# Optimization experiments

Hardware: AMD Instinct MI355X
Metric: run time of the kernel (lower is better)

Reference implementation:

```python
import jax, jax.numpy as jnp
import numpy as np
from jax import lax

TAU = 1.0
HIDDEN = 512
OUT = 12
BATCH = 8192
STEPS = 256


def setup_inputs() -> dict:
    key = jax.random.key(0)
    k = jax.random.split(key, 6)
    scale = 1.0 / np.sqrt(HIDDEN)
    return {
        "x": jax.random.normal(k[0], (BATCH, 1), dtype=jnp.float32),
        "T": STEPS,
        "I_w": jax.random.normal(k[1], (HIDDEN, 1), dtype=jnp.float32) * scale,
        "H_w": jax.random.normal(k[2], (HIDDEN, HIDDEN), dtype=jnp.float32) * scale,
        "O_w": jax.random.normal(k[3], (OUT, HIDDEN), dtype=jnp.float32) * scale,
        "v": jax.random.normal(k[4], (HIDDEN,), dtype=jnp.float32) * 0.05,
        "m": jax.random.normal(k[5], (OUT,), dtype=jnp.float32) * 0.05,
    }


def reference(x, T, I_w, H_w, O_w, v, m):
    # x: [B, 1]; I_w: [H, 1]; H_w: [H, H]; O_w: [O, H]
    B = x.shape[0]
    H = H_w.shape[0]
    alpha = 1.0 / TAU
    # x is constant across timesteps, so precompute the input drive once.
    drive = x @ I_w.T + v  # [B, H]

    def step(carry, _):
        u, z = carry
        u = (1.0 - alpha) * u + alpha * (drive + z @ H_w.T)
        z = jnp.tanh(u)
        y = jax.nn.sigmoid(z @ O_w.T + m)  # [B, O]
        return (u, z), y

    u0 = jnp.zeros((B, H), dtype=x.dtype)
    z0 = jnp.zeros((B, H), dtype=x.dtype)
    _, Y = lax.scan(step, (u0, z0), None, length=T)  # Y: [T, B, O]
    return jnp.transpose(Y, (1, 0, 2))  # [B, T, O]
```

## Files before the change

### kernel.cpp

```cpp
#include <hip/hip_runtime.h>

typedef __attribute__((ext_vector_type(4)))  int   int32x4;
typedef __attribute__((ext_vector_type(16))) int   int32x16;
typedef __attribute__((ext_vector_type(16))) float f32x16;
typedef unsigned char uchar;

#define HID 512
#define BT 32
#define OUTN 12

#define SH 0.28125f
#define S_COMB (SH / 16129.0f)

static __device__ __forceinline__ void quant2(float f, int& q1, int& q2) {
    float h  = fminf(fmaxf(f * (1.0f / SH), -1.0f), 1.0f) * 127.0f;
    float Q1 = rintf(h);
    float r1 = (h - Q1) * 128.0f;
    float Q2 = rintf(r1);
    q1 = (int)Q1; q2 = (int)Q2;
}

__global__ void pack_h(const float* __restrict__ Hw, uchar* __restrict__ Hpk) {
    int t  = blockIdx.x * blockDim.x + threadIdx.x;
    int l  = t & 63;
    int L  = (t >> 6) & 1;
    int ks = (t >> 7) & 15;
    int w  = t >> 11;
    int n  = w * 32 + (l & 31);
    int k0 = ks * 32 + (l >> 5) * 16;
    uint d[4] = {0, 0, 0, 0};
#pragma unroll
    for (int j = 0; j < 16; ++j) {
        int q1, q2;
        quant2(Hw[n * HID + k0 + j], q1, q2);
        int q = L ? q2 : q1;
        d[j >> 2] |= ((uint)(q & 255)) << (8 * (j & 3));
    }
    *(uint4*)(Hpk + (size_t)t * 16) = make_uint4(d[0], d[1], d[2], d[3]);
}

__global__ void pack_o(const float* __restrict__ Ow, uchar* __restrict__ Opk) {
    int t  = blockIdx.x * blockDim.x + threadIdx.x;
    int l  = t & 63;
    int ks = (t >> 6) & 7;
    int L  = t >> 9;
    int o  = l & 15;
    int k0 = ks * 64 + (l >> 4) * 16;
    uint d[4] = {0, 0, 0, 0};
#pragma unroll
    for (int j = 0; j < 16; ++j) {
        float f = (o < OUTN) ? Ow[o * HID + k0 + j] : 0.0f;
        int q1, q2;
        quant2(f, q1, q2);
        int q = L ? q2 : q1;
        d[j >> 2] |= ((uint)(q & 255)) << (8 * (j & 3));
    }
    *(uint4*)(Opk + (size_t)t * 16) = make_uint4(d[0], d[1], d[2], d[3]);
}


static __device__ __forceinline__ void out_gemm(const char* zr, const uchar* __restrict__ Opk,
                                                const float* mbv, int wloc, int l,
                                                float* __restrict__ out,
                                                int b0, int trow, int T) {
    int32x4 aA = {0, 0, 0, 0}, aB = {0, 0, 0, 0};
    const int m     = l & 15;
    const int om    = wloc * 16 + m;
    const int obase = om * 512;
    const int oxor  = (om & 15) << 4;
    const int okb   = (l >> 4) * 16;
    const uchar* op = Opk + (size_t)l * 16;
#pragma unroll
    for (int ks = 0; ks < 8; ++ks) {
        int32x4 o1 = *(const int32x4*)(op + ks * 1024);
        int32x4 o2 = *(const int32x4*)(op + 8192 + ks * 1024);
        int off = obase + ((ks * 64 + okb) ^ oxor);
        int32x4 z1 = *(const int32x4*)(zr + off);
        int32x4 z2 = *(const int32x4*)(zr + 16384 + off);
        aA = __builtin_amdgcn_mfma_i32_16x16x64_i8(o1, z1, aA, 0, 0, 0);
        aB = __builtin_amdgcn_mfma_i32_16x16x64_i8(o1, z2, aB, 0, 0, 0);
        aB = __builtin_amdgcn_mfma_i32_16x16x64_i8(o2, z1, aB, 0, 0, 0);
    }
    if ((l >> 4) < 3) {
        float4 y4;
        float* yp = &y4.x;
#pragma unroll
        for (int r = 0; r < 4; ++r) {
            float logit = mbv[r] + S_COMB * ((float)aA[r] + 0.0078125f * (float)aB[r]);
            yp[r] = __fdividef(1.0f, 1.0f + __expf(-logit));
        }
        *(float4*)(out + ((size_t)(b0 + om) * T + trow) * OUTN + (l >> 4) * 4) = y4;
    }
}

__launch_bounds__(1024, 4)
__global__ void ctrnn_kernel(const float* __restrict__ x,
                             const int*   __restrict__ Tp,
                             const float* __restrict__ Iw,
                             const float* __restrict__ v,
                             const float* __restrict__ mb,
                             const uchar* __restrict__ Hpk,
                             const uchar* __restrict__ Opk,
                             float* __restrict__ out) {
    __shared__ uint4 zs4[4096];
    char* zsc = (char*)zs4;

    const int T   = Tp[0];
    const int tid = threadIdx.x;
    const int l   = tid & 63;
    const int w   = tid >> 6;
    const int b0  = blockIdx.x * BT;

#pragma unroll
    for (int i = 0; i < 2; ++i) zs4[tid + i * 1024] = make_uint4(0, 0, 0, 0);

    const float xm = x[b0 + (l & 31)];
    f32x16 drv;
#pragma unroll
    for (int r = 0; r < 16; ++r) {
        int n = w * 32 + (r & 3) + 8 * (r >> 2) + 4 * (l >> 5);
        drv[r] = fmaf(xm, Iw[n], v[n]);
    }

    float mbv[4] = {0.f, 0.f, 0.f, 0.f};
    if ((l >> 4) < 3) {
#pragma unroll
        for (int r = 0; r < 4; ++r) mbv[r] = mb[(l >> 4) * 4 + r];
    }

    const uchar* hp = Hpk + (size_t)(w * 16) * 2048 + (size_t)l * 16;

    const int am    = l & 31;
    const int abase = am * 512;
    const int axor  = (am & 15) << 4;
    const int akb   = (l >> 5) * 16;

    __syncthreads();

    for (int t = 0; t < T; ++t) {
        const char* zr = zsc + (t & 1) * 32768;
        char*       zw = zsc + ((t & 1) ^ 1) * 32768;

        if (((w & 14) == ((t & 7) * 2)) && t > 0)
            out_gemm(zr, Opk, mbv, w & 1, l, out, b0, t - 1, T);

        int32x16 a2 = {0}, a3 = {0};
#pragma unroll 4
        for (int ks = 0; ks < 16; ++ks) {
            const uchar* hk = hp + (size_t)ks * 2048;
            int32x4 h1 = *(const int32x4*)(hk);
            int32x4 h2 = *(const int32x4*)(hk + 1024);
            int off = abase + ((ks * 32 + akb) ^ axor);
            int32x4 z1 = *(const int32x4*)(zr + off);
            int32x4 z2 = *(const int32x4*)(zr + 16384 + off);
            a2 = __builtin_amdgcn_mfma_i32_32x32x32_i8(h1, z1, a2, 0, 0, 0);
            a3 = __builtin_amdgcn_mfma_i32_32x32x32_i8(h1, z2, a3, 0, 0, 0);
            a3 = __builtin_amdgcn_mfma_i32_32x32x32_i8(h2, z1, a3, 0, 0, 0);
        }

        {
            const int h5 = l >> 5;
#pragma unroll
            for (int rq = 0; rq < 4; ++rq) {
                uint d1 = 0, d2 = 0;
#pragma unroll
                for (int e = 0; e < 4; ++e) {
                    int r = rq * 4 + e;
                    float s = (float)a2[r] + 0.0078125f * (float)a3[r];
                    float u = fmaf(S_COMB, s, drv[r]);
                    float ex = __expf(2.0f * u);
                    float z  = 1.0f - __fdividef(2.0f, ex + 1.0f);
                    float h  = z * 127.0f;
                    float Q1 = rintf(h);
                    float r1 = (h - Q1) * 128.0f;
                    float Q2 = rintf(r1);
                    d1 |= ((uint)((int)Q1 & 255)) << (8 * e);
                    d2 |= ((uint)((int)Q2 & 255)) << (8 * e);
                }
                int nb  = w * 32 + 8 * rq + 4 * h5;
                int off = abase + (nb ^ axor);
                *(uint*)(zw + off)         = d1;
                *(uint*)(zw + 16384 + off) = d2;
            }
        }
        __syncthreads();
    }

    if (w < 2)
        out_gemm(zsc + (T & 1) * 32768, Opk, mbv, w, l, out, b0, T - 1, T);
}

extern "C" void kernel_launch(void* const* d_in, const int* in_sizes, int n_in,
                              void* d_out, int out_size, void* d_ws, size_t ws_size,
                              hipStream_t stream) {
    const float* x  = (const float*)d_in[0];
    const int*   T  = (const int*)d_in[1];
    const float* Iw = (const float*)d_in[2];
    const float* Hw = (const float*)d_in[3];
    const float* Ow = (const float*)d_in[4];
    const float* v  = (const float*)d_in[5];
    const float* m  = (const float*)d_in[6];
    float* out = (float*)d_out;

    uchar* Hpk = (uchar*)d_ws;
    uchar* Opk = Hpk + 524288;

    pack_h<<<dim3(128), dim3(256), 0, stream>>>(Hw, Hpk);
    pack_o<<<dim3(4),   dim3(256), 0, stream>>>(Ow, Opk);
    ctrnn_kernel<<<dim3(256), dim3(1024), 0, stream>>>(x, T, Iw, v, m, Hpk, Opk, out);
}
```

Before: 2.301 ms.

## Keep H weights resident in registers/LDS and stream the rest via async LDS loads

```diff
diff --git a/kernel.cpp b/kernel.cpp
--- a/kernel.cpp
+++ b/kernel.cpp
@@ -59,7 +59,7 @@
 }
 
 
-static __device__ __forceinline__ void out_gemm(const char* zr, const uchar* __restrict__ Opk,
+static __device__ __forceinline__ void out_gemm(const char* zsc, const char* opb,
                                                 const float* mbv, int wloc, int l,
                                                 float* __restrict__ out,
                                                 int b0, int trow, int T) {
@@ -69,14 +69,13 @@
     const int obase = om * 512;
     const int oxor  = (om & 15) << 4;
     const int okb   = (l >> 4) * 16;
-    const uchar* op = Opk + (size_t)l * 16;
 #pragma unroll
     for (int ks = 0; ks < 8; ++ks) {
-        int32x4 o1 = *(const int32x4*)(op + ks * 1024);
-        int32x4 o2 = *(const int32x4*)(op + 8192 + ks * 1024);
+        int32x4 o1 = *(const int32x4*)(opb + ks * 1024 + (size_t)l * 16);
+        int32x4 o2 = *(const int32x4*)(opb + 8192 + ks * 1024 + (size_t)l * 16);
         int off = obase + ((ks * 64 + okb) ^ oxor);
-        int32x4 z1 = *(const int32x4*)(zr + off);
-        int32x4 z2 = *(const int32x4*)(zr + 16384 + off);
+        int32x4 z1 = *(const int32x4*)(zsc + off);
+        int32x4 z2 = *(const int32x4*)(zsc + 16384 + off);
         aA = __builtin_amdgcn_mfma_i32_16x16x64_i8(o1, z1, aA, 0, 0, 0);
         aB = __builtin_amdgcn_mfma_i32_16x16x64_i8(o1, z2, aB, 0, 0, 0);
         aB = __builtin_amdgcn_mfma_i32_16x16x64_i8(o2, z1, aB, 0, 0, 0);
@@ -93,7 +92,58 @@
     }
 }
 
-__launch_bounds__(1024, 4)
+#define ISSUE_SITE(S)                                                                   \
+    {                                                                                   \
+        const int c_   = ((S) + 4) % 28;                                                \
+        const int tt_  = c_ & 1;                                                        \
+        const int kk_  = (c_ < 24) ? (c_ >> 1) : (14 + ((c_ - 24) >> 1));               \
+        const int lvl_ = (c_ < 24) ? 1024 : 0;                                          \
+        const uchar* g_ = Hpk + (size_t)(2 * w + tt_) * 32768 + kk_ * 2048 + lvl_       \
+                          + (size_t)l * 16;                                             \
+        __builtin_amdgcn_global_load_lds(                                               \
+            (const __attribute__((address_space(1))) uint*)g_,                          \
+            (__attribute__((address_space(3))) uint*)(ringb + ((S) & 3) * 1024),        \
+            16, 0, 0);                                                                  \
+    }
+
+#define WAITV2()                                                \
+    asm volatile("s_waitcnt vmcnt(2)" ::: "memory");            \
+    __builtin_amdgcn_sched_barrier(0)
+
+#define BARRIER()                                               \
+    asm volatile("s_waitcnt lgkmcnt(0)" ::: "memory");          \
+    __builtin_amdgcn_s_barrier();                               \
+    asm volatile("" ::: "memory");                              \
+    __builtin_amdgcn_sched_barrier(0)
+
+#define PHASE2(A2, A3, TAU)                                                             \
+    {                                                                                   \
+        const int h5 = l >> 5;                                                          \
+        _Pragma("unroll")                                                               \
+        for (int rq = 0; rq < 4; ++rq) {                                                \
+            uint d1 = 0, d2 = 0;                                                        \
+            _Pragma("unroll")                                                           \
+            for (int e = 0; e < 4; ++e) {                                               \
+                int r = rq * 4 + e;                                                     \
+                float s = (float)(A2)[r] + 0.0078125f * (float)(A3)[r];                 \
+                float u = fmaf(S_COMB, s, (TAU) ? drv1[r] : drv0[r]);                   \
+                float ex = __expf(2.0f * u);                                            \
+                float z  = 1.0f - __fdividef(2.0f, ex + 1.0f);                          \
+                float h  = z * 127.0f;                                                  \
+                float Q1 = rintf(h);                                                    \
+                float r1 = (h - Q1) * 128.0f;                                           \
+                float Q2 = rintf(r1);                                                   \
+                d1 |= ((uint)((int)Q1 & 255)) << (8 * e);                               \
+                d2 |= ((uint)((int)Q2 & 255)) << (8 * e);                               \
+            }                                                                           \
+            int nb  = w * 64 + (TAU) * 32 + 8 * rq + 4 * h5;                            \
+            int off = abase + (nb ^ axor);                                              \
+            *(uint*)(zsc + off)         = d1;                                           \
+            *(uint*)(zsc + 16384 + off) = d2;                                           \
+        }                                                                               \
+    }
+
+__launch_bounds__(512)
 __global__ void ctrnn_kernel(const float* __restrict__ x,
                              const int*   __restrict__ Tp,
                              const float* __restrict__ Iw,
@@ -102,7 +152,7 @@
                              const uchar* __restrict__ Hpk,
                              const uchar* __restrict__ Opk,
                              float* __restrict__ out) {
-    __shared__ uint4 zs4[4096];
+    __shared__ uint4 zs4[9216];
     char* zsc = (char*)zs4;
 
     const int T   = Tp[0];
@@ -111,15 +161,41 @@
     const int w   = tid >> 6;
     const int b0  = blockIdx.x * BT;
 
-#pragma unroll
-    for (int i = 0; i < 2; ++i) zs4[tid + i * 1024] = make_uint4(0, 0, 0, 0);
+    char* ringb = zsc + 114688 + w * 4096;
+    const char* opb = zsc + 98304;
+
+#pragma unroll
+    for (int i = 0; i < 4; ++i) zs4[tid + i * 512] = make_uint4(0, 0, 0, 0);
+
+#pragma unroll
+    for (int tau = 0; tau < 2; ++tau)
+#pragma unroll
+        for (int i = 0; i < 4; ++i) {
+            const uchar* src = Hpk + (size_t)(2 * w + tau) * 32768 + (12 + i) * 2048
+                               + 1024 + (size_t)l * 16;
+            *(uint4*)(zsc + 32768 + (size_t)(w * 8 + tau * 4 + i) * 1024 + (size_t)l * 16)
+                = *(const uint4*)src;
+        }
+
+#pragma unroll
+    for (int i = 0; i < 2; ++i)
+        ((uint4*)(zsc + 98304))[tid + i * 512] = ((const uint4*)Opk)[tid + i * 512];
+
+    int32x4 h1R0[14], h1R1[14];
+#pragma unroll
+    for (int ks = 0; ks < 14; ++ks) {
+        h1R0[ks] = *(const int32x4*)(Hpk + (size_t)(2 * w + 0) * 32768 + ks * 2048 + (size_t)l * 16);
+        h1R1[ks] = *(const int32x4*)(Hpk + (size_t)(2 * w + 1) * 32768 + ks * 2048 + (size_t)l * 16);
+    }
 
     const float xm = x[b0 + (l & 31)];
-    f32x16 drv;
+    f32x16 drv0, drv1;
 #pragma unroll
     for (int r = 0; r < 16; ++r) {
-        int n = w * 32 + (r & 3) + 8 * (r >> 2) + 4 * (l >> 5);
-        drv[r] = fmaf(xm, Iw[n], v[n]);
+        int ns = (r & 3) + 8 * (r >> 2) + 4 * (l >> 5);
+        int n0 = w * 64 + ns, n1 = w * 64 + 32 + ns;
+        drv0[r] = fmaf(xm, Iw[n0], v[n0]);
+        drv1[r] = fmaf(xm, Iw[n1], v[n1]);
     }
 
     float mbv[4] = {0.f, 0.f, 0.f, 0.f};
@@ -127,8 +203,6 @@
 #pragma unroll
         for (int r = 0; r < 4; ++r) mbv[r] = mb[(l >> 4) * 4 + r];
     }
-
-    const uchar* hp = Hpk + (size_t)(w * 16) * 2048 + (size_t)l * 16;
 
     const int am    = l & 31;
     const int abase = am * 512;
@@ -137,57 +211,68 @@
 
     __syncthreads();
 
+    ISSUE_SITE(24); ISSUE_SITE(25); ISSUE_SITE(26); ISSUE_SITE(27);
+
+#pragma unroll 1
     for (int t = 0; t < T; ++t) {
-        const char* zr = zsc + (t & 1) * 32768;
-        char*       zw = zsc + ((t & 1) ^ 1) * 32768;
-
-        if (((w & 14) == ((t & 7) * 2)) && t > 0)
-            out_gemm(zr, Opk, mbv, w & 1, l, out, b0, t - 1, T);
-
-        int32x16 a2 = {0}, a3 = {0};
-#pragma unroll 4
+        if (((w >> 1) == (t & 3)) && t > 0)
+            out_gemm(zsc, opb, mbv, w & 1, l, out, b0, t - 1, T);
+
+        int32x16 a2t0 = {0}, a3t0 = {0}, a2t1 = {0}, a3t1 = {0};
+#pragma unroll
         for (int ks = 0; ks < 16; ++ks) {
-            const uchar* hk = hp + (size_t)ks * 2048;
-            int32x4 h1 = *(const int32x4*)(hk);
-            int32x4 h2 = *(const int32x4*)(hk + 1024);
             int off = abase + ((ks * 32 + akb) ^ axor);
-            int32x4 z1 = *(const int32x4*)(zr + off);
-            int32x4 z2 = *(const int32x4*)(zr + 16384 + off);
-            a2 = __builtin_amdgcn_mfma_i32_32x32x32_i8(h1, z1, a2, 0, 0, 0);
-            a3 = __builtin_amdgcn_mfma_i32_32x32x32_i8(h1, z2, a3, 0, 0, 0);
-            a3 = __builtin_amdgcn_mfma_i32_32x32x32_i8(h2, z1, a3, 0, 0, 0);
+            int32x4 z1 = *(const int32x4*)(zsc + off);
+            int32x4 z2 = *(const int32x4*)(zsc + 16384 + off);
+
+            int32x4 h2a, h2b, h1a, h1b;
+            if (ks <= 11) {
+                WAITV2();
+                h2a = *(const int32x4*)(ringb + ((2 * ks) & 3) * 1024 + (size_t)l * 16);
+                h2b = *(const int32x4*)(ringb + ((2 * ks + 1) & 3) * 1024 + (size_t)l * 16);
+            } else {
+                int i = ks - 12;
+                h2a = *(const int32x4*)(zsc + 32768 + (size_t)(w * 8 + i) * 1024 + (size_t)l * 16);
+                h2b = *(const int32x4*)(zsc + 32768 + (size_t)(w * 8 + 4 + i) * 1024 + (size_t)l * 16);
+            }
+            if (ks >= 14) {
+                WAITV2();
+                int s0 = 24 + (ks - 14) * 2;
+                h1a = *(const int32x4*)(ringb + (s0 & 3) * 1024 + (size_t)l * 16);
+                h1b = *(const int32x4*)(ringb + ((s0 + 1) & 3) * 1024 + (size_t)l * 16);
+            } else {
+                h1a = h1R0[ks];
+                h1b = h1R1[ks];
+            }
+
+            a2t0 = __builtin_amdgcn_mfma_i32_32x32x32_i8(h1a, z1, a2t0, 0, 0, 0);
+            a3t0 = __builtin_amdgcn_mfma_i32_32x32x32_i8(h1a, z2, a3t0, 0, 0, 0);
+            a3t0 = __builtin_amdgcn_mfma_i32_32x32x32_i8(h2a, z1, a3t0, 0, 0, 0);
+            a2t1 = __builtin_amdgcn_mfma_i32_32x32x32_i8(h1b, z1, a2t1, 0, 0, 0);
+            a3t1 = __builtin_amdgcn_mfma_i32_32x32x32_i8(h1b, z2, a3t1, 0, 0, 0);
+            a3t1 = __builtin_amdgcn_mfma_i32_32x32x32_i8(h2b, z1, a3t1, 0, 0, 0);
+
+            if (ks <= 11) {
+                __builtin_amdgcn_sched_barrier(0);
+                ISSUE_SITE(2 * ks); ISSUE_SITE(2 * ks + 1);
+            }
+            if (ks >= 14) {
+                __builtin_amdgcn_sched_barrier(0);
+                int s0 = 24 + (ks - 14) * 2;
+                ISSUE_SITE(s0); ISSUE_SITE(s0 + 1);
+            }
         }
 
-        {
-            const int h5 = l >> 5;
-#pragma unroll
-            for (int rq = 0; rq < 4; ++rq) {
-                uint d1 = 0, d2 = 0;
-#pragma unroll
-                for (int e = 0; e < 4; ++e) {
-                    int r = rq * 4 + e;
-                    float s = (float)a2[r] + 0.0078125f * (float)a3[r];
-                    float u = fmaf(S_COMB, s, drv[r]);
-                    float ex = __expf(2.0f * u);
-                    float z  = 1.0f - __fdividef(2.0f, ex + 1.0f);
-                    float h  = z * 127.0f;
-                    float Q1 = rintf(h);
-                    float r1 = (h - Q1) * 128.0f;
-                    float Q2 = rintf(r1);
-                    d1 |= ((uint)((int)Q1 & 255)) << (8 * e);
-                    d2 |= ((uint)((int)Q2 & 255)) << (8 * e);
-                }
-                int nb  = w * 32 + 8 * rq + 4 * h5;
-                int off = abase + (nb ^ axor);
-                *(uint*)(zw + off)         = d1;
-                *(uint*)(zw + 16384 + off) = d2;
-            }
-        }
-        __syncthreads();
+        BARRIER();
+
+        PHASE2(a2t0, a3t0, 0);
+        PHASE2(a2t1, a3t1, 1);
+
+        BARRIER();
     }
 
     if (w < 2)
-        out_gemm(zsc + (T & 1) * 32768, Opk, mbv, w, l, out, b0, T - 1, T);
+        out_gemm(zsc, opb, mbv, w, l, out, b0, T - 1, T);
 }
 
 extern "C" void kernel_launch(void* const* d_in, const int* in_sizes, int n_in,
@@ -207,5 +292,5 @@
 
     pack_h<<<dim3(128), dim3(256), 0, stream>>>(Hw, Hpk);
     pack_o<<<dim3(4),   dim3(256), 0, stream>>>(Ow, Opk);
-    ctrnn_kernel<<<dim3(256), dim3(1024), 0, stream>>>(x, T, Iw, v, m, Hpk, Opk, out);
-}
+    ctrnn_kernel<<<dim3(256), dim3(512), 0, stream>>>(x, T, Iw, v, m, Hpk, Opk, out);
+}
```

Result: slower. 4.558 ms (+98.1%).

## Stream recurrent weights through per-wave LDS ring with async global_load_lds

Applied to the files above, without the earlier changes.

```diff
diff --git a/kernel.cpp b/kernel.cpp
--- a/kernel.cpp
+++ b/kernel.cpp
@@ -59,7 +59,7 @@
 }
 
 
-static __device__ __forceinline__ void out_gemm(const char* zr, const uchar* __restrict__ Opk,
+static __device__ __forceinline__ void out_gemm(const char* zr, const char* opb,
                                                 const float* mbv, int wloc, int l,
                                                 float* __restrict__ out,
                                                 int b0, int trow, int T) {
@@ -69,7 +69,7 @@
     const int obase = om * 512;
     const int oxor  = (om & 15) << 4;
     const int okb   = (l >> 4) * 16;
-    const uchar* op = Opk + (size_t)l * 16;
+    const char* op  = opb + (size_t)l * 16;
 #pragma unroll
     for (int ks = 0; ks < 8; ++ks) {
         int32x4 o1 = *(const int32x4*)(op + ks * 1024);
@@ -93,7 +93,30 @@
     }
 }
 
-__launch_bounds__(1024, 4)
+#define ISSUE_SITE(S)                                                                   \
+    {                                                                                   \
+        const int c_  = ((S) + 4) & 31;                                                 \
+        const int kk_ = c_ >> 1;                                                        \
+        const int LL_ = c_ & 1;                                                         \
+        const uchar* g_ = Hpk + (size_t)(w * 16 + kk_) * 2048 + LL_ * 1024              \
+                          + (size_t)l * 16;                                             \
+        __builtin_amdgcn_global_load_lds(                                               \
+            (const __attribute__((address_space(1))) uint*)g_,                          \
+            (__attribute__((address_space(3))) uint*)(ringb + ((S) & 3) * 1024),        \
+            16, 0, 0);                                                                  \
+    }
+
+#define WAITV2()                                                \
+    asm volatile("s_waitcnt vmcnt(2)" ::: "memory");            \
+    __builtin_amdgcn_sched_barrier(0)
+
+#define BARRIER()                                               \
+    asm volatile("s_waitcnt lgkmcnt(0)" ::: "memory");          \
+    __builtin_amdgcn_s_barrier();                               \
+    asm volatile("" ::: "memory");                              \
+    __builtin_amdgcn_sched_barrier(0)
+
+__launch_bounds__(1024)
 __global__ void ctrnn_kernel(const float* __restrict__ x,
                              const int*   __restrict__ Tp,
                              const float* __restrict__ Iw,
@@ -102,7 +125,7 @@
                              const uchar* __restrict__ Hpk,
                              const uchar* __restrict__ Opk,
                              float* __restrict__ out) {
-    __shared__ uint4 zs4[4096];
+    __shared__ uint4 zs4[10240];
     char* zsc = (char*)zs4;
 
     const int T   = Tp[0];
@@ -111,8 +134,13 @@
     const int w   = tid >> 6;
     const int b0  = blockIdx.x * BT;
 
+    char* ringb = zsc + 98304 + w * 4096;
+    const char* opb = zsc + 65536;
+
 #pragma unroll
     for (int i = 0; i < 2; ++i) zs4[tid + i * 1024] = make_uint4(0, 0, 0, 0);
+
+    ((uint4*)(zsc + 65536))[tid] = ((const uint4*)Opk)[tid];
 
     const float xm = x[b0 + (l & 31)];
     f32x16 drv;
@@ -127,8 +155,6 @@
 #pragma unroll
         for (int r = 0; r < 4; ++r) mbv[r] = mb[(l >> 4) * 4 + r];
     }
-
-    const uchar* hp = Hpk + (size_t)(w * 16) * 2048 + (size_t)l * 16;
 
     const int am    = l & 31;
     const int abase = am * 512;
@@ -137,25 +163,31 @@
 
     __syncthreads();
 
+    ISSUE_SITE(28); ISSUE_SITE(29); ISSUE_SITE(30); ISSUE_SITE(31);
+
+#pragma unroll 1
     for (int t = 0; t < T; ++t) {
         const char* zr = zsc + (t & 1) * 32768;
         char*       zw = zsc + ((t & 1) ^ 1) * 32768;
 
         if (((w & 14) == ((t & 7) * 2)) && t > 0)
-            out_gemm(zr, Opk, mbv, w & 1, l, out, b0, t - 1, T);
+            out_gemm(zr, opb, mbv, w & 1, l, out, b0, t - 1, T);
 
         int32x16 a2 = {0}, a3 = {0};
-#pragma unroll 4
+#pragma unroll
         for (int ks = 0; ks < 16; ++ks) {
-            const uchar* hk = hp + (size_t)ks * 2048;
-            int32x4 h1 = *(const int32x4*)(hk);
-            int32x4 h2 = *(const int32x4*)(hk + 1024);
+            WAITV2();
+            int32x4 h1 = *(const int32x4*)(ringb + ((2 * ks) & 3) * 1024 + (size_t)l * 16);
+            int32x4 h2 = *(const int32x4*)(ringb + ((2 * ks + 1) & 3) * 1024 + (size_t)l * 16);
             int off = abase + ((ks * 32 + akb) ^ axor);
             int32x4 z1 = *(const int32x4*)(zr + off);
             int32x4 z2 = *(const int32x4*)(zr + 16384 + off);
             a2 = __builtin_amdgcn_mfma_i32_32x32x32_i8(h1, z1, a2, 0, 0, 0);
             a3 = __builtin_amdgcn_mfma_i32_32x32x32_i8(h1, z2, a3, 0, 0, 0);
             a3 = __builtin_amdgcn_mfma_i32_32x32x32_i8(h2, z1, a3, 0, 0, 0);
+            __builtin_amdgcn_sched_barrier(0);
+            ISSUE_SITE(2 * ks);
+            ISSUE_SITE(2 * ks + 1);
         }
 
         {
@@ -183,11 +215,12 @@
                 *(uint*)(zw + 16384 + off) = d2;
             }
         }
-        __syncthreads();
-    }
-
+        BARRIER();
+    }
+
+    asm volatile("s_waitcnt vmcnt(0)" ::: "memory");
     if (w < 2)
-        out_gemm(zsc + (T & 1) * 32768, Opk, mbv, w, l, out, b0, T - 1, T);
+        out_gemm(zsc + (T & 1) * 32768, opb, mbv, w, l, out, b0, T - 1, T);
 }
 
 extern "C" void kernel_launch(void* const* d_in, const int* in_sizes, int n_in,
```

Result: slower. 3.190 ms (+38.6%).
